# Kernel tuning notes

Measured on AMD Instinct MI355X. Metric: run time of the kernel, lower is better.

## Reference

```python
import jax, jax.numpy as jnp
from jax import lax
import numpy as np

B, N, C = 64, 8732, 81  # batch, anchors (SSD300), classes (COCO+bg)
POS_RATE = 0.003        # keep 3*num_pos < N (argsort column index must be in range)


def setup_inputs() -> dict:
    key = jax.random.key(0)
    k1, k2, k3, k4, k5, k6 = jax.random.split(key, 6)
    pred_conf = jax.random.normal(k1, (B, N, C), dtype=jnp.float32)
    pred_loc = jax.random.normal(k2, (B, N, 4), dtype=jnp.float32)
    # one-hot gt_conf; class 0 = background; sparse positives
    is_pos = jax.random.uniform(k3, (B, N)) < POS_RATE
    labels = jnp.where(is_pos, jax.random.randint(k4, (B, N), 1, C), 0)
    gt_conf = jax.nn.one_hot(labels, C, dtype=jnp.float32)
    gt_loc = jax.random.normal(k5, (B, N, 4), dtype=jnp.float32)
    return {"pred_conf": pred_conf, "pred_loc": pred_loc,
            "gt_conf": gt_conf, "gt_loc": gt_loc}


def reference(pred_conf, pred_loc, gt_conf, gt_loc):
    negative_ratio = 3.0
    # softmax cross entropy per anchor: [B, N]
    log_sm = jax.nn.log_softmax(pred_conf, axis=-1)
    conf_loss = -jnp.sum(log_sm * gt_conf, axis=-1)

    # positive mask (gt background prob == 0 => positive); detached in original
    pos_mask = (lax.stop_gradient(gt_conf)[:, :, 0] == 0).astype(jnp.float32)
    num_pos = jnp.sum(pos_mask)
    positive_conf_loss = pos_mask * conf_loss

    # hard-negative mining (faithful to original, including the quirk that the
    # "threshold" is the argsort INDEX value at column num_negative_conf)
    neg_mask = 1.0 - pos_mask
    cl_neg = lax.stop_gradient(conf_loss) * neg_mask  # detached in original
    order = jnp.argsort(cl_neg, axis=-1)              # [B, N] ascending
    num_neg = (negative_ratio * num_pos).astype(jnp.int32)  # scalar, traced
    idx = jnp.broadcast_to(num_neg, (cl_neg.shape[0], 1))
    thr = jnp.take_along_axis(order, idx, axis=1).astype(jnp.float32)  # [B,1]
    neg_mask = neg_mask * (cl_neg > thr).astype(jnp.float32)
    negative_conf_loss = neg_mask * conf_loss

    conf_total = jnp.sum(positive_conf_loss + negative_conf_loss, axis=-1)  # [B]

    # smooth-L1-ish loc loss (faithful, incl. loc_loss_mask == linear mask bug)
    d = pred_loc - gt_loc
    lin = (jnp.abs(lax.stop_gradient(d)) > 1.0).astype(jnp.float32)
    loc = ((jnp.abs(d) - 0.5) * lin + 0.5 * d * d * (1.0 - lin)) * lin
    loc_total = jnp.sum(loc, axis=(-1, -2))  # [B]

    return conf_total, loc_total
```

## Files before the change

### kernel.cpp

```cpp
#include <hip/hip_runtime.h>
#include <hip/hip_bf16.h>
#include <math.h>

#define NCLS 81
#define NANCH 8732
#define NB 64
#define BUCKET_STRIDE 16

__global__ __launch_bounds__(256) void conf_kernel(
    const float* __restrict__ pred_conf,
    const float* __restrict__ gt_conf,
    float* __restrict__ cl_out,
    int* __restrict__ pos_buckets,
    float* __restrict__ row_pos)
{
    const int tid = threadIdx.x;
    const int anchor = blockIdx.x * 64 + (tid >> 2);
    const int q = tid & 3;
    const float* xrow = pred_conf + (size_t)anchor * NCLS;
    const float* grow = gt_conf + (size_t)anchor * NCLS;

    float x[21];
    float m = -INFINITY;
#pragma unroll
    for (int j = 0; j < 21; ++j) {
        int c = q + 4 * j;
        x[j] = (c < NCLS) ? xrow[c] : -INFINITY;
        m = fmaxf(m, x[j]);
    }
    m = fmaxf(m, __shfl_xor(m, 1));
    m = fmaxf(m, __shfl_xor(m, 2));

    float s = 0.f;
#pragma unroll
    for (int j = 0; j < 21; ++j) {
        int c = q + 4 * j;
        if (c < NCLS) s += expf(x[j] - m);
    }
    s += __shfl_xor(s, 1);
    s += __shfl_xor(s, 2);
    const float lse = m + logf(s);

    float dot = 0.f, g0 = 1.f;
#pragma unroll
    for (int j = 0; j < 21; ++j) {
        int c = q + 4 * j;
        if (c < NCLS) {
            float g = grow[c];
            if (c == 0) g0 = g;
            dot = fmaf(g, x[j] - lse, dot);
        }
    }
    dot += __shfl_xor(dot, 1);
    dot += __shfl_xor(dot, 2);
    const float conf_loss = -dot;

    const bool posf = (q == 0) && (g0 == 0.0f);
    if (q == 0) cl_out[anchor] = posf ? 0.0f : conf_loss;

    const int b = anchor / NANCH;
    const float contrib = posf ? conf_loss : 0.0f;
    const int bF = __builtin_amdgcn_readfirstlane(b);
    float c0 = (b == bF) ? contrib : 0.0f;
    float c1 = contrib - c0;
    for (int off = 32; off; off >>= 1) {
        c0 += __shfl_xor(c0, off);
        c1 += __shfl_xor(c1, off);
    }
    const int pc = (int)__popcll(__ballot(posf));
    if ((tid & 63) == 0) {
        if (c0 != 0.f) atomicAdd(&row_pos[bF], c0);
        if (c1 != 0.f) atomicAdd(&row_pos[bF + 1], c1);
        if (pc) atomicAdd(&pos_buckets[(blockIdx.x & 63) * BUCKET_STRIDE], pc);
    }
}

__global__ __launch_bounds__(256) void loc_kernel(
    const float* __restrict__ pred_loc,
    const float* __restrict__ gt_loc,
    float* __restrict__ out)
{
    __shared__ float red[4];
    const int b = blockIdx.y;
    const int idx = blockIdx.x * 256 + threadIdx.x;
    float local = 0.f;
    if (idx < NANCH) {
        const float4* p = (const float4*)(pred_loc + (long long)b * (NANCH * 4));
        const float4* g = (const float4*)(gt_loc + (long long)b * (NANCH * 4));
        float4 pv = p[idx];
        float4 gv = g[idx];
        float a0 = fabsf(pv.x - gv.x), a1 = fabsf(pv.y - gv.y);
        float a2 = fabsf(pv.z - gv.z), a3 = fabsf(pv.w - gv.w);
        local  = (a0 > 1.f) ? (a0 - 0.5f) : 0.f;
        local += (a1 > 1.f) ? (a1 - 0.5f) : 0.f;
        local += (a2 > 1.f) ? (a2 - 0.5f) : 0.f;
        local += (a3 > 1.f) ? (a3 - 0.5f) : 0.f;
    }
    for (int off = 32; off; off >>= 1) local += __shfl_xor(local, off);
    if ((threadIdx.x & 63) == 0) red[threadIdx.x >> 6] = local;
    __syncthreads();
    if (threadIdx.x == 0)
        atomicAdd(&out[64 + b], red[0] + red[1] + red[2] + red[3]);
}

__global__ __launch_bounds__(1024) void select_kernel(
    const float* __restrict__ val,
    const int* __restrict__ pos_buckets,
    const float* __restrict__ row_pos,
    float* __restrict__ out)
{
    __shared__ float cl[NANCH];
    __shared__ int hist[256];
    __shared__ int wsum[16];
    __shared__ float fred[16];
    __shared__ int sh_numpos;
    __shared__ unsigned int sh_prefix;
    __shared__ int sh_k, sh_thr;

    const int b = blockIdx.x;
    const int tid = threadIdx.x;
    const int lane = tid & 63, w = tid >> 6;
    const float* row = val + b * NANCH;

    if (tid < 64) {
        int v = pos_buckets[tid * BUCKET_STRIDE];
        for (int off = 32; off; off >>= 1) v += __shfl_xor(v, off);
        if (tid == 0) sh_numpos = v;
    }
    for (int i = tid; i < NANCH; i += 1024) cl[i] = row[i];
    __syncthreads();

    int k = 3 * sh_numpos;
    if (k > NANCH - 1) k = NANCH - 1;
    if (k < 0) k = 0;

    unsigned int prefix = 0u;
    for (int r = 0; r < 4; ++r) {
        const int shift = 24 - 8 * r;
        const unsigned int maskHigh = (r == 0) ? 0u : (0xFFFFFFFFu << (shift + 8));
        if (tid < 256) hist[tid] = 0;
        __syncthreads();
        for (int i = tid; i < NANCH; i += 1024) {
            unsigned int u = __float_as_uint(cl[i]);
            if ((u & maskHigh) == prefix)
                atomicAdd(&hist[(u >> shift) & 0xFF], 1);
        }
        __syncthreads();
        int h = 0, v = 0;
        if (tid < 256) {
            h = hist[tid];
            v = h;
#pragma unroll
            for (int off = 1; off < 64; off <<= 1) {
                int u2 = __shfl_up(v, off);
                if (lane >= off) v += u2;
            }
            if (lane == 63) wsum[w] = v;
        }
        __syncthreads();
        if (tid < 256) {
            int add = 0;
            for (int i = 0; i < w; ++i) add += wsum[i];
            int incl = v + add, excl = incl - h;
            if (excl <= k && k < incl) {
                sh_prefix = prefix | ((unsigned int)tid << shift);
                sh_k = k - excl;
            }
        }
        __syncthreads();
        prefix = sh_prefix;
        k = sh_k;
        __syncthreads();
    }
    const unsigned int T = prefix;

    const int CHUNK = 9;
    int lo = tid * CHUNK; if (lo > NANCH) lo = NANCH;
    int hi = lo + CHUNK; if (hi > NANCH) hi = NANCH;
    int cnt = 0;
    for (int i = lo; i < hi; ++i)
        cnt += (__float_as_uint(cl[i]) == T);
    int v2 = cnt;
#pragma unroll
    for (int off = 1; off < 64; off <<= 1) {
        int u2 = __shfl_up(v2, off);
        if (lane >= off) v2 += u2;
    }
    if (lane == 63) wsum[w] = v2;
    __syncthreads();
    if (tid < 16) {
        int s = wsum[tid];
#pragma unroll
        for (int off = 1; off < 16; off <<= 1) {
            int u2 = __shfl_up(s, off);
            if (lane >= off) s += u2;
        }
        wsum[tid] = s;
    }
    __syncthreads();
    {
        int add = (w == 0) ? 0 : wsum[w - 1];
        int incl = v2 + add, excl = incl - cnt;
        if (excl <= k && k < incl) {
            int need = k - excl, idx = NANCH - 1;
            for (int i = lo; i < hi; ++i) {
                if (__float_as_uint(cl[i]) == T) {
                    if (need == 0) { idx = i; break; }
                    --need;
                }
            }
            sh_thr = idx;
        }
    }
    __syncthreads();

    const float thr = (float)sh_thr;
    float local = 0.f;
    for (int i = tid; i < NANCH; i += 1024) {
        float c = cl[i];
        if (c > thr) local += c;
    }
    for (int off = 32; off; off >>= 1) local += __shfl_xor(local, off);
    if (lane == 0) fred[w] = local;
    __syncthreads();
    if (tid == 0) {
        float t = row_pos[b];
        for (int i = 0; i < 16; ++i) t += fred[i];
        out[b] = t;
    }
}

extern "C" void kernel_launch(void* const* d_in, const int* in_sizes, int n_in,
                              void* d_out, int out_size, void* d_ws, size_t ws_size,
                              hipStream_t stream) {
    const float* pred_conf = (const float*)d_in[0];
    const float* pred_loc  = (const float*)d_in[1];
    const float* gt_conf   = (const float*)d_in[2];
    const float* gt_loc    = (const float*)d_in[3];
    float* out = (float*)d_out;

    int*   pos_buckets = (int*)d_ws;
    float* row_pos     = (float*)((char*)d_ws + 4096);
    float* vals        = (float*)((char*)d_ws + 8192);

    hipMemsetAsync(d_ws, 0, 8192, stream);
    hipMemsetAsync(d_out, 0, 128 * sizeof(float), stream);

    conf_kernel<<<NB * NANCH / 64, 256, 0, stream>>>(pred_conf, gt_conf, vals,
                                                     pos_buckets, row_pos);
    loc_kernel<<<dim3((NANCH + 255) / 256, NB), 256, 0, stream>>>(pred_loc, gt_loc, out);
    select_kernel<<<NB, 1024, 0, stream>>>(vals, pos_buckets, row_pos, out);
}
```

Before: 404.3 us.

## Stage conf tiles in LDS, derive labels from one-hot, warp-aggregate histogram atomics

The conf kernel now loads each 64-anchor tile of pred_conf into LDS with direct global-to-LDS float4 loads. It scans gt_conf with coalesced float4 reads to find the nonzero label per anchor, so the loss becomes lse minus the logit at that label instead of a full dot product. The select kernel's radix histogram now aggregates same-bin updates inside each wavefront before the shared atomic. This targets the strided per-anchor row loads and atomic contention. It assumes gt_conf is strictly one-hot (exactly one nonzero per row) and adds a block-wide barrier.

```diff
diff --git a/kernel.cpp b/kernel.cpp
--- a/kernel.cpp
+++ b/kernel.cpp
@@ -6,6 +6,8 @@
 #define NANCH 8732
 #define NB 64
 #define BUCKET_STRIDE 16
+#define TILE_F 5184
+#define TILE_F4 1296
 
 __global__ __launch_bounds__(256) void conf_kernel(
     const float* __restrict__ pred_conf,
@@ -14,18 +16,60 @@
     int* __restrict__ pos_buckets,
     float* __restrict__ row_pos)
 {
+    __shared__ float sx[TILE_F];
+    __shared__ int label_s[64];
+    __shared__ int pcnt[4];
+
     const int tid = threadIdx.x;
-    const int anchor = blockIdx.x * 64 + (tid >> 2);
+    const int lane = tid & 63, wid = tid >> 6;
+    const size_t tbase = (size_t)blockIdx.x * TILE_F;
+    const float4* p4 = (const float4*)(pred_conf + tbase);
+    const float4* g4 = (const float4*)(gt_conf + tbase);
+
+    for (int c = wid; c < 21; c += 4) {
+        int f4 = c * 64 + lane;
+        if (f4 < TILE_F4) {
+            __builtin_amdgcn_global_load_lds(
+                (const __attribute__((address_space(1))) unsigned int*)(p4 + f4),
+                (__attribute__((address_space(3))) unsigned int*)(&sx[f4 * 4]),
+                16, 0, 0);
+        }
+    }
+
+    int mycnt = 0;
+#pragma unroll
+    for (int i = 0; i < 6; ++i) {
+        int k = tid + 256 * i;
+        if (k < TILE_F4) {
+            float4 g = g4[k];
+            int base = 4 * k;
+            float gv[4] = {g.x, g.y, g.z, g.w};
+#pragma unroll
+            for (int t = 0; t < 4; ++t) {
+                if (gv[t] != 0.0f) {
+                    int gidx = base + t;
+                    int a = gidx / NCLS;
+                    int cls = gidx - a * NCLS;
+                    label_s[a] = cls;
+                    mycnt += (cls != 0);
+                }
+            }
+        }
+    }
+    for (int off = 32; off; off >>= 1) mycnt += __shfl_xor(mycnt, off);
+    if (lane == 0) pcnt[wid] = mycnt;
+
+    __syncthreads();
+
+    const int a = tid >> 2;
     const int q = tid & 3;
-    const float* xrow = pred_conf + (size_t)anchor * NCLS;
-    const float* grow = gt_conf + (size_t)anchor * NCLS;
-
-    float x[21];
-    float m = -INFINITY;
+    const float* xr = sx + a * NCLS;
+
+    float x[21], m = -INFINITY;
 #pragma unroll
     for (int j = 0; j < 21; ++j) {
         int c = q + 4 * j;
-        x[j] = (c < NCLS) ? xrow[c] : -INFINITY;
+        x[j] = (c < NCLS) ? xr[c] : -INFINITY;
         m = fmaxf(m, x[j]);
     }
     m = fmaxf(m, __shfl_xor(m, 1));
@@ -41,22 +85,15 @@
     s += __shfl_xor(s, 2);
     const float lse = m + logf(s);
 
-    float dot = 0.f, g0 = 1.f;
-#pragma unroll
-    for (int j = 0; j < 21; ++j) {
-        int c = q + 4 * j;
-        if (c < NCLS) {
-            float g = grow[c];
-            if (c == 0) g0 = g;
-            dot = fmaf(g, x[j] - lse, dot);
-        }
-    }
-    dot += __shfl_xor(dot, 1);
-    dot += __shfl_xor(dot, 2);
-    const float conf_loss = -dot;
-
-    const bool posf = (q == 0) && (g0 == 0.0f);
-    if (q == 0) cl_out[anchor] = posf ? 0.0f : conf_loss;
+    const int anchor = blockIdx.x * 64 + a;
+    float conf_loss = 0.f;
+    bool posf = false;
+    if (q == 0) {
+        int lbl = label_s[a];
+        conf_loss = lse - xr[lbl];
+        posf = (lbl != 0);
+        cl_out[anchor] = posf ? 0.0f : conf_loss;
+    }
 
     const int b = anchor / NANCH;
     const float contrib = posf ? conf_loss : 0.0f;
@@ -67,11 +104,13 @@
         c0 += __shfl_xor(c0, off);
         c1 += __shfl_xor(c1, off);
     }
-    const int pc = (int)__popcll(__ballot(posf));
-    if ((tid & 63) == 0) {
+    if (lane == 0) {
         if (c0 != 0.f) atomicAdd(&row_pos[bF], c0);
         if (c1 != 0.f) atomicAdd(&row_pos[bF + 1], c1);
-        if (pc) atomicAdd(&pos_buckets[(blockIdx.x & 63) * BUCKET_STRIDE], pc);
+    }
+    if (tid == 0) {
+        int tot = pcnt[0] + pcnt[1] + pcnt[2] + pcnt[3];
+        if (tot) atomicAdd(&pos_buckets[(blockIdx.x & 63) * BUCKET_STRIDE], tot);
     }
 }
 
@@ -140,10 +179,20 @@
         const unsigned int maskHigh = (r == 0) ? 0u : (0xFFFFFFFFu << (shift + 8));
         if (tid < 256) hist[tid] = 0;
         __syncthreads();
-        for (int i = tid; i < NANCH; i += 1024) {
-            unsigned int u = __float_as_uint(cl[i]);
-            if ((u & maskHigh) == prefix)
-                atomicAdd(&hist[(u >> shift) & 0xFF], 1);
+        for (int i0 = 0; i0 < 9216; i0 += 1024) {
+            int i = i0 + tid;
+            unsigned int u = (i < NANCH) ? __float_as_uint(cl[i]) : 0u;
+            bool valid = (i < NANCH) && ((u & maskHigh) == prefix);
+            int bin = (int)((u >> shift) & 0xFF);
+            unsigned long long act = __ballot(valid);
+            while (act) {
+                int leader = (int)__ffsll(act) - 1;
+                int lbin = __shfl(bin, leader);
+                unsigned long long sm = __ballot(valid && bin == lbin);
+                if (lane == leader) atomicAdd(&hist[lbin], (int)__popcll(sm));
+                act &= ~sm;
+                if (valid && bin == lbin) valid = false;
+            }
         }
         __syncthreads();
         int h = 0, v = 0;
@@ -246,8 +295,8 @@
     hipMemsetAsync(d_ws, 0, 8192, stream);
     hipMemsetAsync(d_out, 0, 128 * sizeof(float), stream);
 
-    conf_kernel<<<NB * NANCH / 64, 256, 0, stream>>>(pred_conf, gt_conf, vals,
-                                                     pos_buckets, row_pos);
+    conf_kernel<<<NANCH, 256, 0, stream>>>(pred_conf, gt_conf, vals,
+                                           pos_buckets, row_pos);
     loc_kernel<<<dim3((NANCH + 255) / 256, NB), 256, 0, stream>>>(pred_loc, gt_loc, out);
     select_kernel<<<NB, 1024, 0, stream>>>(vals, pos_buckets, row_pos, out);
 }
```

Measured after the change: 462.3 us. 1.14x slower.
